# Kernel tuning notes

Measured on AMD Instinct MI355X. Metric: run time of the kernel, lower is better.

## Reference

```python
import jax, jax.numpy as jnp
import numpy as np

D_MODEL = 1024
NUM_HEADS = 16
HEAD_DIM = D_MODEL // NUM_HEADS
B, T = 2, 2048


def setup_inputs() -> dict:
    key = jax.random.key(0)
    kx, kq, kk, kv, ko = jax.random.split(key, 5)
    s = 1.0 / np.sqrt(D_MODEL)  # ~Linear init scale
    return {
        "x": jax.random.normal(kx, (B, T, D_MODEL), dtype=jnp.float32),
        "Wq": jax.random.normal(kq, (D_MODEL, D_MODEL), dtype=jnp.float32) * s,
        "Wk": jax.random.normal(kk, (D_MODEL, D_MODEL), dtype=jnp.float32) * s,
        "Wv": jax.random.normal(kv, (D_MODEL, D_MODEL), dtype=jnp.float32) * s,
        "Wo": jax.random.normal(ko, (D_MODEL, D_MODEL), dtype=jnp.float32) * s,
    }


def reference(x, Wq, Wk, Wv, Wo):
    Bc, Tc, _ = x.shape
    H, D = NUM_HEADS, HEAD_DIM
    scale = jnp.sqrt(jnp.asarray(D, x.dtype))
    # torch Linear (bias=False): y = x @ W^T
    q = (x @ Wq.T).reshape(Bc, Tc, H, D).transpose(0, 2, 1, 3)  # [B,H,T,D]
    k = (x @ Wk.T).reshape(Bc, Tc, H, D).transpose(0, 2, 1, 3)
    v = (x @ Wv.T).reshape(Bc, Tc, H, D).transpose(0, 2, 1, 3)
    scores = jnp.einsum("bhtd,bhsd->bhts", q, k) / scale  # [B,H,T,T]
    # causal bias: upper triangle (strictly future positions) gets -1e9
    causal_bias = jnp.triu(jnp.ones((Tc, Tc), dtype=jnp.float32), k=1) * -1e9
    scores = scores + causal_bias
    weights = jax.nn.softmax(scores, axis=-1)
    # dropout is identity in eval / p=0
    out = jnp.einsum("bhts,bhsd->bhtd", weights, v)  # [B,H,T,D]
    out = out.transpose(0, 2, 1, 3).reshape(Bc, Tc, H * D)
    return out @ Wo.T
```

## Files before the change

kernel.cpp:

```cpp
#include <hip/hip_runtime.h>
#include <hip/hip_bf16.h>

typedef __bf16 bf16_t;
typedef __bf16 bf16x2 __attribute__((ext_vector_type(2)));
typedef __bf16 bf16x4 __attribute__((ext_vector_type(4)));
typedef __bf16 bf16x8 __attribute__((ext_vector_type(8)));
typedef float  f32x4  __attribute__((ext_vector_type(4)));

#define D_MODEL 1024
#define HEADS   16
#define HD      64
#define BB      2
#define TT      2048
#define MROWS   (BB*TT)

#define GLDS16(g, l) __builtin_amdgcn_global_load_lds( \
    (const __attribute__((address_space(1))) void*)(g), \
    (__attribute__((address_space(3))) void*)(l), 16, 0, 0)

static __device__ __forceinline__ int pack_bf16(float a, float b) {
    bf16x2 t; t[0] = (bf16_t)a; t[1] = (bf16_t)b;
    return __builtin_bit_cast(int, t);
}

__global__ __launch_bounds__(256) void cvt_all_kernel(const float* __restrict__ x,
                                                      const float* __restrict__ wq,
                                                      const float* __restrict__ wk,
                                                      const float* __restrict__ wv,
                                                      const float* __restrict__ wo,
                                                      bf16_t* __restrict__ dst) {
    const int i = blockIdx.x * 256 + threadIdx.x;
    const float* src;
    int s;
    if (i < 1048576) { src = x; s = i; }
    else {
        int j = i - 1048576;
        int w = j >> 18;
        s = j & 262143;
        src = (w == 0) ? wq : (w == 1) ? wk : (w == 2) ? wv : wo;
    }
    float4 v = reinterpret_cast<const float4*>(src)[s];
    bf16x4 o;
    o[0] = (bf16_t)v.x; o[1] = (bf16_t)v.y; o[2] = (bf16_t)v.z; o[3] = (bf16_t)v.w;
    reinterpret_cast<bf16x4*>(dst)[i] = o;
}

template<int MODE, int BN>
__global__ __launch_bounds__(256) void gemm_bt(const bf16_t* __restrict__ A,
                                               const bf16_t* __restrict__ Bw,
                                               void* __restrict__ Cout,
                                               int M, int N, int K) {
    constexpr int NI = BN / 32;
    __shared__ __align__(16) bf16_t As[128*32];
    __shared__ __align__(16) bf16_t Bs[BN*32];
    const int tid   = threadIdx.x;
    const int lane  = tid & 63;
    const int wave  = tid >> 6;
    const int col16 = lane & 15;
    const int quad  = lane >> 4;
    const int wrow  = (wave & 1) * 64;
    const int wcol  = (wave >> 1) * (BN / 2);
    const int bm    = blockIdx.y * 128;
    const int bn    = blockIdx.x * BN;

    const int lr = tid >> 2;
    const int lc = (tid & 3) * 8;

    const bf16_t* agp = &A [(size_t)(bm + lr)*K + lc];
    const bf16_t* bgp = &Bw[(size_t)(bn + lr)*K + lc];
    const size_t half = (size_t)64 * K;
    bf16_t* as_lo = &As[wave*512];
    bf16_t* as_hi = &As[2048 + wave*512];
    bf16_t* bs_lo = &Bs[wave*512];
    bf16_t* bs_hi = &Bs[2048 + wave*512];

    f32x4 acc[4][NI];
#pragma unroll
    for (int i = 0; i < 4; i++)
#pragma unroll
        for (int j = 0; j < NI; j++) acc[i][j] = (f32x4){0.f, 0.f, 0.f, 0.f};

    for (int k0 = 0; k0 < K; k0 += 32) {
        GLDS16(agp + k0,        as_lo);
        GLDS16(agp + half + k0, as_hi);
        GLDS16(bgp + k0,        bs_lo);
        if (BN == 128) GLDS16(bgp + half + k0, bs_hi);
        __syncthreads();

        bf16x8 af[4], bfr[NI];
#pragma unroll
        for (int mi = 0; mi < 4; mi++)
            af[mi] = *reinterpret_cast<const bf16x8*>(&As[(wrow + mi*16 + col16)*32 + quad*8]);
#pragma unroll
        for (int ni = 0; ni < NI; ni++)
            bfr[ni] = *reinterpret_cast<const bf16x8*>(&Bs[(wcol + ni*16 + col16)*32 + quad*8]);
#pragma unroll
        for (int mi = 0; mi < 4; mi++)
#pragma unroll
            for (int ni = 0; ni < NI; ni++)
                acc[mi][ni] = __builtin_amdgcn_mfma_f32_16x16x32_bf16(af[mi], bfr[ni], acc[mi][ni], 0, 0, 0);
        __syncthreads();
    }

#pragma unroll
    for (int mi = 0; mi < 4; mi++) {
#pragma unroll
        for (int r = 0; r < 4; r++) {
            const int gm = bm + wrow + mi*16 + quad*4 + r;
            const int t  = gm & (TT - 1);
            const int b  = gm >> 11;
#pragma unroll
            for (int ni = 0; ni < NI; ni++) {
                const int gn = bn + wcol + ni*16 + col16;
                float v = acc[mi][ni][r];
                if (MODE == 2) {
                    reinterpret_cast<float*>(Cout)[(size_t)gm * N + gn] = v;
                } else {
                    const int which = gn >> 10;
                    if (which == 0) v *= 0.18033688f;
                    const int n = gn & 1023;
                    const int h = n >> 6, d = n & 63;
                    const size_t off = (size_t)(which == 2 ? 3 : which) * MROWS * D_MODEL;
                    bf16_t* base = reinterpret_cast<bf16_t*>(Cout) + off;
                    base[(((size_t)(b*HEADS + h))*TT + t)*HD + d] = (bf16_t)v;
                }
            }
        }
    }
}

__global__ __launch_bounds__(256) void transpose_v(const bf16_t* __restrict__ V,
                                                   bf16_t* __restrict__ Vt) {
    __shared__ bf16_t tile[64][72];
    const int tid = threadIdx.x;
    const int bh = blockIdx.y;
    const int t0 = blockIdx.x * 64;
    const bf16_t* src = V + ((size_t)bh * TT + t0) * HD;
#pragma unroll
    for (int i = 0; i < 2; i++) {
        const int r = i*32 + (tid >> 3), c = (tid & 7) * 8;
        *reinterpret_cast<bf16x8*>(&tile[r][c]) =
            *reinterpret_cast<const bf16x8*>(&src[(size_t)r * HD + c]);
    }
    __syncthreads();
    bf16_t* dst = Vt + (size_t)bh * HD * TT + t0;
#pragma unroll
    for (int i = 0; i < 2; i++) {
        const int d = i*32 + (tid >> 3), tc = (tid & 7) * 8;
        bf16x8 o;
#pragma unroll
        for (int j = 0; j < 8; j++) o[j] = tile[tc + j][d];
        *reinterpret_cast<bf16x8*>(&dst[(size_t)d * TT + tc]) = o;
    }
}

__global__ __launch_bounds__(256, 5) void attn_kernel(const bf16_t* __restrict__ Q,
                                                      const bf16_t* __restrict__ Kk,
                                                      const bf16_t* __restrict__ Vt,
                                                      bf16_t* __restrict__ O) {
    __shared__ __align__(16) bf16_t Ks[2][64*64];
    __shared__ __align__(16) bf16_t Vs[2][64*64];

    const int tid   = threadIdx.x;
    const int lane  = tid & 63;
    const int wave  = tid >> 6;
    const int col16 = lane & 15;
    const int quad  = lane >> 4;

    const int bx = blockIdx.x;
    const int r_ = bx >> 8, s_ = bx & 255;
    const int bh = s_ & 31;
    const int qt = (r_ == 0) ? (24 + (s_ >> 5))
                             : ((r_ - 1) * 8 + 7 - (s_ >> 5));
    const int qb    = qt * 64;
    const int qbase = qb + wave * 16;
    const int nkt   = qt + 1;

    const bf16_t* Qb = Q  + (size_t)bh * TT * HD;
    const bf16_t* Kb = Kk + (size_t)bh * TT * HD;
    const bf16_t* Vb = Vt + (size_t)bh * HD * TT;

    bf16x8 qf0 = *reinterpret_cast<const bf16x8*>(&Qb[(size_t)(qbase + col16)*HD + quad*8]);
    bf16x8 qf1 = *reinterpret_cast<const bf16x8*>(&Qb[(size_t)(qbase + col16)*HD + 32 + quad*8]);

    const int srow = (tid >> 3) & 31;
    const int sg   = ((lane & 7) ^ (srow & 7)) * 8;

    auto stage = [&](int kt, int buf) {
        const int s0 = kt * 64;
        GLDS16(&Kb[(size_t)(s0 + srow)*HD + sg],        &Ks[buf][wave*512]);
        GLDS16(&Kb[(size_t)(s0 + srow + 32)*HD + sg],   &Ks[buf][2048 + wave*512]);
        GLDS16(&Vb[(size_t)srow*TT + s0 + sg],          &Vs[buf][wave*512]);
        GLDS16(&Vb[(size_t)(srow + 32)*TT + s0 + sg],   &Vs[buf][2048 + wave*512]);
    };

    f32x4 acc[4];
#pragma unroll
    for (int i = 0; i < 4; i++) acc[i] = (f32x4){0.f,0.f,0.f,0.f};
    float lsum = 0.f;

    const int x7 = col16 & 7;
    const int a1 = ((quad & 1) * 32 + col16) * 4;
    const int a2 = a1 + 64;
    const bool hi = quad >= 2;

    stage(0, 0);
    __syncthreads();

    for (int kt = 0; kt < nkt; kt++) {
        const int buf = kt & 1;
        if (kt + 1 < nkt) stage(kt + 1, buf ^ 1);
        const int s0 = kt * 64;
        const bool diag = (kt == nkt - 1);

        int pk[4][2];
#pragma unroll
        for (int c = 0; c < 4; c++) {
            bf16x8 k0 = *reinterpret_cast<const bf16x8*>(
                &Ks[buf][(c*16 + col16)*64 + ((0*4 + quad) ^ x7)*8]);
            bf16x8 k1 = *reinterpret_cast<const bf16x8*>(
                &Ks[buf][(c*16 + col16)*64 + ((1*4 + quad) ^ x7)*8]);
            f32x4 sv = __builtin_amdgcn_mfma_f32_16x16x32_bf16(k0, qf0, (f32x4){0.f,0.f,0.f,0.f}, 0, 0, 0);
            sv       = __builtin_amdgcn_mfma_f32_16x16x32_bf16(k1, qf1, sv, 0, 0, 0);

            float pr[4];
#pragma unroll
            for (int r = 0; r < 4; r++) pr[r] = exp2f(sv[r]);
            if (diag) {
#pragma unroll
                for (int r = 0; r < 4; r++)
                    if (s0 + c*16 + quad*4 + r > qbase + col16) pr[r] = 0.f;
            }
            lsum += (pr[0] + pr[1]) + (pr[2] + pr[3]);
            pk[c][0] = pack_bf16(pr[0], pr[1]);
            pk[c][1] = pack_bf16(pr[2], pr[3]);
        }

#pragma unroll
        for (int kc = 0; kc < 2; kc++) {
            int b0l = __builtin_amdgcn_ds_bpermute(a1, pk[2*kc][0]);
            int b0h = __builtin_amdgcn_ds_bpermute(a1, pk[2*kc+1][0]);
            int b1l = __builtin_amdgcn_ds_bpermute(a1, pk[2*kc][1]);
            int b1h = __builtin_amdgcn_ds_bpermute(a1, pk[2*kc+1][1]);
            int b2l = __builtin_amdgcn_ds_bpermute(a2, pk[2*kc][0]);
            int b2h = __builtin_amdgcn_ds_bpermute(a2, pk[2*kc+1][0]);
            int b3l = __builtin_amdgcn_ds_bpermute(a2, pk[2*kc][1]);
            int b3h = __builtin_amdgcn_ds_bpermute(a2, pk[2*kc+1][1]);
            int4 bi = { hi ? b0h : b0l, hi ? b1h : b1l, hi ? b2h : b2l, hi ? b3h : b3l };
            bf16x8 pf = __builtin_bit_cast(bf16x8, bi);
#pragma unroll
            for (int c = 0; c < 4; c++) {
                bf16x8 vf = *reinterpret_cast<const bf16x8*>(
                    &Vs[buf][(c*16 + col16)*64 + ((kc*4 + quad) ^ x7)*8]);
                acc[c] = __builtin_amdgcn_mfma_f32_16x16x32_bf16(vf, pf, acc[c], 0, 0, 0);
            }
        }
        __syncthreads();
    }

    float l = lsum;
    l += __shfl_xor(l, 16);
    l += __shfl_xor(l, 32);
    const float inv = 1.0f / l;

    const int b_ = bh >> 4, h = bh & 15;
    const int t = qbase + col16;
    bf16_t* Ob = &O[(((size_t)(b_*TT + t))*HEADS + h)*HD + quad*4];
#pragma unroll
    for (int c = 0; c < 4; c++) {
        bf16x4 o4;
#pragma unroll
        for (int r = 0; r < 4; r++) o4[r] = (bf16_t)(acc[c][r] * inv);
        *reinterpret_cast<bf16x4*>(&Ob[c*16]) = o4;
    }
}

extern "C" void kernel_launch(void* const* d_in, const int* in_sizes, int n_in,
                              void* d_out, int out_size, void* d_ws, size_t ws_size,
                              hipStream_t stream) {
    const float* x  = (const float*)d_in[0];
    const float* Wq = (const float*)d_in[1];
    const float* Wk = (const float*)d_in[2];
    const float* Wv = (const float*)d_in[3];
    const float* Wo = (const float*)d_in[4];
    float* out = (float*)d_out;

    bf16_t* Xb  = (bf16_t*)d_ws;
    bf16_t* Wqb = Xb  + (size_t)MROWS * D_MODEL;
    bf16_t* Wob = Wqb + (size_t)3 * D_MODEL * D_MODEL;
    bf16_t* Qw  = Wob + (size_t)D_MODEL * D_MODEL;
    bf16_t* Kw  = Qw  + (size_t)MROWS * D_MODEL;
    bf16_t* Vt  = Kw  + (size_t)MROWS * D_MODEL;
    bf16_t* Ow  = Vt  + (size_t)MROWS * D_MODEL;

    cvt_all_kernel<<<(MROWS*D_MODEL + 4*D_MODEL*D_MODEL) / 4 / 256, 256, 0, stream>>>(
        x, Wq, Wk, Wv, Wo, Xb);

    dim3 gqkv(3 * D_MODEL / 128, MROWS / 128);
    gemm_bt<0,128><<<gqkv, 256, 0, stream>>>(Xb, Wqb, Qw, MROWS, 3 * D_MODEL, D_MODEL);

    dim3 gt(TT / 64, BB * HEADS);
    transpose_v<<<gt, 256, 0, stream>>>(Ow, Vt);

    attn_kernel<<<dim3(1024), 256, 0, stream>>>(Qw, Kw, Vt, Ow);

    dim3 go(D_MODEL / 64, MROWS / 128);
    gemm_bt<2,64><<<go, 256, 0, stream>>>(Ow, Wob, out, MROWS, D_MODEL, D_MODEL);
}
```

Baseline: 191.7 us.

## Split attention waves across key halves and query pairs with LDS reduction

Reorganizes the attention kernel's wave work split. Each wave now handles 32 query rows and half of each 64-key tile, instead of 16 query rows against the full tile. The aim is to reuse each K and V fragment read from shared memory across two query groups, cutting LDS reads per MFMA. In exchange, the partial output accumulators and row sums must be merged through shared memory at the end with an extra barrier, register pressure rises, and the occupancy hint drops from 5 to 4.

```diff
diff --git a/kernel.cpp b/kernel.cpp
--- a/kernel.cpp
+++ b/kernel.cpp
@@ -154,7 +154,7 @@
     }
 }
 
-__global__ __launch_bounds__(256, 5) void attn_kernel(const bf16_t* __restrict__ Q,
+__global__ __launch_bounds__(256, 4) void attn_kernel(const bf16_t* __restrict__ Q,
                                                       const bf16_t* __restrict__ Kk,
                                                       const bf16_t* __restrict__ Vt,
                                                       bf16_t* __restrict__ O) {
@@ -166,6 +166,8 @@
     const int wave  = tid >> 6;
     const int col16 = lane & 15;
     const int quad  = lane >> 4;
+    const int kw    = wave & 1;
+    const int qw    = wave >> 1;
 
     const int bx = blockIdx.x;
     const int r_ = bx >> 8, s_ = bx & 255;
@@ -173,15 +175,20 @@
     const int qt = (r_ == 0) ? (24 + (s_ >> 5))
                              : ((r_ - 1) * 8 + 7 - (s_ >> 5));
     const int qb    = qt * 64;
-    const int qbase = qb + wave * 16;
+    const int qbase = qb + qw * 32;
     const int nkt   = qt + 1;
 
     const bf16_t* Qb = Q  + (size_t)bh * TT * HD;
     const bf16_t* Kb = Kk + (size_t)bh * TT * HD;
     const bf16_t* Vb = Vt + (size_t)bh * HD * TT;
 
-    bf16x8 qf0 = *reinterpret_cast<const bf16x8*>(&Qb[(size_t)(qbase + col16)*HD + quad*8]);
-    bf16x8 qf1 = *reinterpret_cast<const bf16x8*>(&Qb[(size_t)(qbase + col16)*HD + 32 + quad*8]);
+    bf16x8 qf[2][2];
+#pragma unroll
+    for (int qg = 0; qg < 2; qg++)
+#pragma unroll
+        for (int h = 0; h < 2; h++)
+            qf[qg][h] = *reinterpret_cast<const bf16x8*>(
+                &Qb[(size_t)(qbase + qg*16 + col16)*HD + h*32 + quad*8]);
 
     const int srow = (tid >> 3) & 31;
     const int sg   = ((lane & 7) ^ (srow & 7)) * 8;
@@ -194,10 +201,12 @@
         GLDS16(&Vb[(size_t)(srow + 32)*TT + s0 + sg],   &Vs[buf][2048 + wave*512]);
     };
 
-    f32x4 acc[4];
-#pragma unroll
-    for (int i = 0; i < 4; i++) acc[i] = (f32x4){0.f,0.f,0.f,0.f};
-    float lsum = 0.f;
+    f32x4 acc[4][2];
+#pragma unroll
+    for (int i = 0; i < 4; i++)
+#pragma unroll
+        for (int j = 0; j < 2; j++) acc[i][j] = (f32x4){0.f,0.f,0.f,0.f};
+    float lsum[2] = {0.f, 0.f};
 
     const int x7 = col16 & 7;
     const int a1 = ((quad & 1) * 32 + col16) * 4;
@@ -213,65 +222,101 @@
         const int s0 = kt * 64;
         const bool diag = (kt == nkt - 1);
 
-        int pk[4][2];
+        bf16x8 k0[2], k1[2];
+#pragma unroll
+        for (int c = 0; c < 2; c++) {
+            k0[c] = *reinterpret_cast<const bf16x8*>(
+                &Ks[buf][(kw*32 + c*16 + col16)*64 + ((0*4 + quad) ^ x7)*8]);
+            k1[c] = *reinterpret_cast<const bf16x8*>(
+                &Ks[buf][(kw*32 + c*16 + col16)*64 + ((1*4 + quad) ^ x7)*8]);
+        }
+
+        int pk[2][2][2];
+#pragma unroll
+        for (int c = 0; c < 2; c++) {
+#pragma unroll
+            for (int qg = 0; qg < 2; qg++) {
+                f32x4 sv = __builtin_amdgcn_mfma_f32_16x16x32_bf16(k0[c], qf[qg][0], (f32x4){0.f,0.f,0.f,0.f}, 0, 0, 0);
+                sv       = __builtin_amdgcn_mfma_f32_16x16x32_bf16(k1[c], qf[qg][1], sv, 0, 0, 0);
+
+                float pr[4];
+#pragma unroll
+                for (int r = 0; r < 4; r++) pr[r] = exp2f(sv[r]);
+                if (diag) {
+#pragma unroll
+                    for (int r = 0; r < 4; r++)
+                        if (s0 + kw*32 + c*16 + quad*4 + r > qbase + qg*16 + col16) pr[r] = 0.f;
+                }
+                lsum[qg] += (pr[0] + pr[1]) + (pr[2] + pr[3]);
+                pk[c][qg][0] = pack_bf16(pr[0], pr[1]);
+                pk[c][qg][1] = pack_bf16(pr[2], pr[3]);
+            }
+        }
+
+        bf16x8 pf[2];
+#pragma unroll
+        for (int qg = 0; qg < 2; qg++) {
+            int b0l = __builtin_amdgcn_ds_bpermute(a1, pk[0][qg][0]);
+            int b0h = __builtin_amdgcn_ds_bpermute(a1, pk[1][qg][0]);
+            int b1l = __builtin_amdgcn_ds_bpermute(a1, pk[0][qg][1]);
+            int b1h = __builtin_amdgcn_ds_bpermute(a1, pk[1][qg][1]);
+            int b2l = __builtin_amdgcn_ds_bpermute(a2, pk[0][qg][0]);
+            int b2h = __builtin_amdgcn_ds_bpermute(a2, pk[1][qg][0]);
+            int b3l = __builtin_amdgcn_ds_bpermute(a2, pk[0][qg][1]);
+            int b3h = __builtin_amdgcn_ds_bpermute(a2, pk[1][qg][1]);
+            int4 bi = { hi ? b0h : b0l, hi ? b1h : b1l, hi ? b2h : b2l, hi ? b3h : b3l };
+            pf[qg] = __builtin_bit_cast(bf16x8, bi);
+        }
 #pragma unroll
         for (int c = 0; c < 4; c++) {
-            bf16x8 k0 = *reinterpret_cast<const bf16x8*>(
-                &Ks[buf][(c*16 + col16)*64 + ((0*4 + quad) ^ x7)*8]);
-            bf16x8 k1 = *reinterpret_cast<const bf16x8*>(
-                &Ks[buf][(c*16 + col16)*64 + ((1*4 + quad) ^ x7)*8]);
-            f32x4 sv = __builtin_amdgcn_mfma_f32_16x16x32_bf16(k0, qf0, (f32x4){0.f,0.f,0.f,0.f}, 0, 0, 0);
-            sv       = __builtin_amdgcn_mfma_f32_16x16x32_bf16(k1, qf1, sv, 0, 0, 0);
-
-            float pr[4];
-#pragma unroll
-            for (int r = 0; r < 4; r++) pr[r] = exp2f(sv[r]);
-            if (diag) {
-#pragma unroll
-                for (int r = 0; r < 4; r++)
-                    if (s0 + c*16 + quad*4 + r > qbase + col16) pr[r] = 0.f;
+            bf16x8 vf = *reinterpret_cast<const bf16x8*>(
+                &Vs[buf][(c*16 + col16)*64 + ((kw*4 + quad) ^ x7)*8]);
+            acc[c][0] = __builtin_amdgcn_mfma_f32_16x16x32_bf16(vf, pf[0], acc[c][0], 0, 0, 0);
+            acc[c][1] = __builtin_amdgcn_mfma_f32_16x16x32_bf16(vf, pf[1], acc[c][1], 0, 0, 0);
+        }
+        __syncthreads();
+    }
+
+#pragma unroll
+    for (int qg = 0; qg < 2; qg++) {
+        lsum[qg] += __shfl_xor(lsum[qg], 16);
+        lsum[qg] += __shfl_xor(lsum[qg], 32);
+    }
+
+    float* Mq = qw ? reinterpret_cast<float*>(&Vs[0][0])
+                   : reinterpret_cast<float*>(&Ks[0][0]);
+    float* LS = reinterpret_cast<float*>(&Vs[0][0]) + 32*68;
+
+    if (kw == 1) {
+#pragma unroll
+        for (int c = 0; c < 4; c++)
+#pragma unroll
+            for (int qg = 0; qg < 2; qg++)
+                *reinterpret_cast<f32x4*>(&Mq[(qg*16 + col16)*68 + c*16 + quad*4]) = acc[c][qg];
+        if (lane < 16) {
+            LS[qw*32 + lane]      = lsum[0];
+            LS[qw*32 + 16 + lane] = lsum[1];
+        }
+    }
+    __syncthreads();
+
+    if (kw == 0) {
+        const int b_ = bh >> 4, h = bh & 15;
+#pragma unroll
+        for (int qg = 0; qg < 2; qg++) {
+            const float l   = lsum[qg] + LS[qw*32 + qg*16 + col16];
+            const float inv = 1.0f / l;
+            const int t = qbase + qg*16 + col16;
+            bf16_t* Ob = &O[(((size_t)(b_*TT + t))*HEADS + h)*HD + quad*4];
+#pragma unroll
+            for (int c = 0; c < 4; c++) {
+                f32x4 m = *reinterpret_cast<const f32x4*>(&Mq[(qg*16 + col16)*68 + c*16 + quad*4]);
+                bf16x4 o4;
+#pragma unroll
+                for (int r = 0; r < 4; r++) o4[r] = (bf16_t)((acc[c][qg][r] + m[r]) * inv);
+                *reinterpret_cast<bf16x4*>(&Ob[c*16]) = o4;
             }
-            lsum += (pr[0] + pr[1]) + (pr[2] + pr[3]);
-            pk[c][0] = pack_bf16(pr[0], pr[1]);
-            pk[c][1] = pack_bf16(pr[2], pr[3]);
-        }
-
-#pragma unroll
-        for (int kc = 0; kc < 2; kc++) {
-            int b0l = __builtin_amdgcn_ds_bpermute(a1, pk[2*kc][0]);
-            int b0h = __builtin_amdgcn_ds_bpermute(a1, pk[2*kc+1][0]);
-            int b1l = __builtin_amdgcn_ds_bpermute(a1, pk[2*kc][1]);
-            int b1h = __builtin_amdgcn_ds_bpermute(a1, pk[2*kc+1][1]);
-            int b2l = __builtin_amdgcn_ds_bpermute(a2, pk[2*kc][0]);
-            int b2h = __builtin_amdgcn_ds_bpermute(a2, pk[2*kc+1][0]);
-            int b3l = __builtin_amdgcn_ds_bpermute(a2, pk[2*kc][1]);
-            int b3h = __builtin_amdgcn_ds_bpermute(a2, pk[2*kc+1][1]);
-            int4 bi = { hi ? b0h : b0l, hi ? b1h : b1l, hi ? b2h : b2l, hi ? b3h : b3l };
-            bf16x8 pf = __builtin_bit_cast(bf16x8, bi);
-#pragma unroll
-            for (int c = 0; c < 4; c++) {
-                bf16x8 vf = *reinterpret_cast<const bf16x8*>(
-                    &Vs[buf][(c*16 + col16)*64 + ((kc*4 + quad) ^ x7)*8]);
-                acc[c] = __builtin_amdgcn_mfma_f32_16x16x32_bf16(vf, pf, acc[c], 0, 0, 0);
-            }
-        }
-        __syncthreads();
-    }
-
-    float l = lsum;
-    l += __shfl_xor(l, 16);
-    l += __shfl_xor(l, 32);
-    const float inv = 1.0f / l;
-
-    const int b_ = bh >> 4, h = bh & 15;
-    const int t = qbase + col16;
-    bf16_t* Ob = &O[(((size_t)(b_*TT + t))*HEADS + h)*HD + quad*4];
-#pragma unroll
-    for (int c = 0; c < 4; c++) {
-        bf16x4 o4;
-#pragma unroll
-        for (int r = 0; r < 4; r++) o4[r] = (bf16_t)(acc[c][r] * inv);
-        *reinterpret_cast<bf16x4*>(&Ob[c*16]) = o4;
+        }
     }
 }
 
```

After: 190.5 us. About the same (-0.6%).
